# Kernel optimization log

Hardware: AMD Instinct MI355X
Metric: run time of the kernel (lower is better)

Reference implementation:

```python
import jax, jax.numpy as jnp
import numpy as np

T, N, E = 64, 50000, 1600000
DYN, STAT, GH, RH = 1, 6, 32, 64


def setup_inputs() -> dict:
    key = jax.random.key(0)
    ks = jax.random.split(key, 12)
    s = 0.05
    return {
        "dyn_seq": jax.random.normal(ks[0], (T, N, DYN), jnp.float32),
        "static": jax.random.normal(ks[1], (N, STAT), jnp.float32),
        "edge_index": jax.random.randint(ks[2], (2, E), 0, N, jnp.int32),
        "gcn_w0": s * jax.random.normal(ks[3], (DYN + STAT, GH), jnp.float32),
        "gcn_b0": jnp.zeros((GH,), jnp.float32),
        "gcn_w1": s * jax.random.normal(ks[4], (GH, GH), jnp.float32),
        "gcn_b1": jnp.zeros((GH,), jnp.float32),
        "w_ih": s * jax.random.normal(ks[5], (3 * RH, GH), jnp.float32),
        "w_hh": s * jax.random.normal(ks[6], (3 * RH, RH), jnp.float32),
        "b_ih": jnp.zeros((3 * RH,), jnp.float32),
        "b_hh": jnp.zeros((3 * RH,), jnp.float32),
        "mlp_w1": s * jax.random.normal(ks[7], (RH, RH), jnp.float32),
        "mlp_b1": jnp.zeros((RH,), jnp.float32),
        "mlp_w2": s * jax.random.normal(ks[8], (1, RH), jnp.float32),
        "mlp_b2": jnp.zeros((1,), jnp.float32),
    }


def reference(dyn_seq, static, edge_index, gcn_w0, gcn_b0, gcn_w1, gcn_b1,
              w_ih, w_hh, b_ih, b_hh, mlp_w1, mlp_b1, mlp_w2, mlp_b2):
    n = static.shape[0]
    # GCNConv normalization (PyG default): add self-loops, sym norm D^-1/2 (A+I) D^-1/2
    loops = jnp.arange(n, dtype=edge_index.dtype)
    src = jnp.concatenate([edge_index[0], loops])
    dst = jnp.concatenate([edge_index[1], loops])
    deg = jax.ops.segment_sum(jnp.ones_like(dst, jnp.float32), dst, num_segments=n)
    dinv = jnp.where(deg > 0, jax.lax.rsqrt(deg), 0.0)
    norm = (dinv[src] * dinv[dst])[:, None]  # [E+N, 1]

    def gcn(h, w, b):
        h = h @ w  # transform first (small feature dim), then aggregate
        agg = jax.ops.segment_sum(h[src] * norm, dst, num_segments=n)
        return jax.nn.relu(agg + b)

    def step(x_t):  # x_t: [N, DYN]
        x = jnp.concatenate([x_t, static], axis=1)
        return gcn(gcn(x, gcn_w0, gcn_b0), gcn_w1, gcn_b1)

    H = jax.lax.map(step, dyn_seq)  # [T, N, GH] (sequential over T to bound memory)

    rh = w_hh.shape[1]

    def gru_step(h, x_t):  # torch nn.GRU cell math
        gx = x_t @ w_ih.T + b_ih
        gh = h @ w_hh.T + b_hh
        xr, xz, xn = jnp.split(gx, 3, axis=-1)
        hr, hz, hn = jnp.split(gh, 3, axis=-1)
        r = jax.nn.sigmoid(xr + hr)
        z = jax.nn.sigmoid(xz + hz)
        cand = jnp.tanh(xn + r * hn)
        h_new = (1.0 - z) * cand + z * h
        return h_new, None

    h0 = jnp.zeros((n, rh), H.dtype)
    h_last, _ = jax.lax.scan(gru_step, h0, H)  # last GRU output == out[:, -1, :]
    hid = jax.nn.relu(h_last @ mlp_w1.T + mlp_b1)
    return (hid @ mlp_w2.T + mlp_b2).squeeze(-1)  # [N]
```

## Files before the change

### kernel.cpp

```cpp
#include <hip/hip_runtime.h>
#include <hip/hip_bf16.h>

#define T_   64
#define N_   50000
#define E_   1600000
#define GH_  32
#define RH_  64
#define TB32_ 32
#define G32B_ 12500
#define GB_  782
#define NB_  196
#define AB_  12500

typedef _Float16 half_t;
typedef __attribute__((ext_vector_type(8))) _Float16 half8;
typedef __attribute__((ext_vector_type(4))) _Float16 half4;
typedef __attribute__((ext_vector_type(4))) float f32x4;
typedef __attribute__((ext_vector_type(4))) int i32x4;

static __device__ __forceinline__ float fast_sigmoid(float v) {
    float e = __expf(-v);
    return __builtin_amdgcn_rcpf(1.0f + e);
}
static __device__ __forceinline__ float fast_tanh(float v) {
    return 2.0f * fast_sigmoid(2.0f * v) - 1.0f;
}


__global__ __launch_bounds__(256)
void k_transpose(const float* __restrict__ dyn, half_t* __restrict__ dynT) {
    __shared__ float tile[64][65];
    int n0 = blockIdx.x * 64;
    int tx = threadIdx.x, ty = threadIdx.y;
#pragma unroll
    for (int r = 0; r < 16; ++r) {
        int t = r * 4 + ty;
        int n = n0 + tx;
        tile[t][tx] = (n < N_) ? dyn[(size_t)t * N_ + n] : 0.0f;
    }
    __syncthreads();
#pragma unroll
    for (int r = 0; r < 16; ++r) {
        int nl = r * 4 + ty;
        int n = n0 + nl;
        if (n < N_) dynT[(size_t)n * 64 + tx] = (half_t)tile[tx][nl];
    }
}

__global__ void k_hist(const int* __restrict__ src, const int* __restrict__ dst,
                       int* __restrict__ cnt) {
    int e = blockIdx.x * blockDim.x + threadIdx.x;
    if (e >= E_) return;
    atomicAdd(&cnt[dst[e] * 16 + (src[e] >> 12)], 1);
}

__global__ __launch_bounds__(256)
void k_scanA(const int* __restrict__ cnt, int* __restrict__ deg,
             int* __restrict__ row_ptr, int* __restrict__ bsum) {
    __shared__ int buf[256];
    int tid = threadIdx.x;
    int i = blockIdx.x * 256 + tid;
    int v = 0;
    if (i < N_) {
        const int4* c4 = (const int4*)(cnt + i * 16);
#pragma unroll
        for (int c = 0; c < 4; ++c) {
            int4 w = c4[c];
            v += w.x + w.y + w.z + w.w;
        }
        deg[i] = v;
    }
    buf[tid] = v;
    __syncthreads();
#pragma unroll
    for (int off = 1; off < 256; off <<= 1) {
        int t = (tid >= off) ? buf[tid - off] : 0;
        __syncthreads();
        buf[tid] += t;
        __syncthreads();
    }
    if (i < N_) row_ptr[i + 1] = buf[tid];
    if (tid == 255) bsum[blockIdx.x] = buf[255];
}
__global__ __launch_bounds__(256)
void k_scanB(int* __restrict__ bsum, int nb) {
    __shared__ int buf[256];
    int tid = threadIdx.x;
    buf[tid] = (tid < nb) ? bsum[tid] : 0;
    __syncthreads();
#pragma unroll
    for (int off = 1; off < 256; off <<= 1) {
        int t = (tid >= off) ? buf[tid - off] : 0;
        __syncthreads();
        buf[tid] += t;
        __syncthreads();
    }
    if (tid < nb) bsum[tid] = (tid > 0) ? buf[tid - 1] : 0;
}
__global__ __launch_bounds__(256)
void k_scanC(int* __restrict__ row_ptr, const int* __restrict__ bsum) {
    int i = blockIdx.x * 256 + threadIdx.x;
    if (i == 0) row_ptr[0] = 0;
    if (i < N_) row_ptr[i + 1] += bsum[blockIdx.x];
}

__global__ __launch_bounds__(256)
void k_rowscan(const int* __restrict__ row_ptr, int* __restrict__ cnt,
               int* __restrict__ rp2) {
    int n = blockIdx.x * 256 + threadIdx.x;
    if (n >= N_) return;
    int run = row_ptr[n];
#pragma unroll
    for (int t = 0; t < 16; ++t) {
        int c = cnt[n * 16 + t];
        rp2[n * 16 + t] = run;
        run += c;
        cnt[n * 16 + t] = 0;
    }
}

__global__ __launch_bounds__(256)
void k_node_init(const int* __restrict__ deg,
                 const float* __restrict__ statics,
                 const float* __restrict__ w0,
                 float* __restrict__ dinv,
                 float* __restrict__ selfn,
                 half_t* __restrict__ h0s) {
    int n = blockIdx.x * blockDim.x + threadIdx.x;
    if (n >= N_) return;
    float d  = (float)deg[n] + 1.0f;
    float di = rsqrtf(d);
    dinv[n] = di;
    selfn[n] = di * di;
    float s[6];
#pragma unroll
    for (int j = 0; j < 6; ++j) s[j] = statics[n * 6 + j];
    half8 o[4];
#pragma unroll
    for (int k = 0; k < GH_; ++k) {
        float v = 0.0f;
#pragma unroll
        for (int j = 0; j < 6; ++j) v += s[j] * w0[(1 + j) * GH_ + k];
        o[k >> 3][k & 7] = (half_t)v;
    }
    half8* dst8 = (half8*)(h0s + (size_t)n * GH_);
#pragma unroll
    for (int c = 0; c < 4; ++c) dst8[c] = o[c];
}

__global__ void k_scatter2(const int* __restrict__ src, const int* __restrict__ dst,
                           const float* __restrict__ dinv,
                           const int* __restrict__ rp2, int* __restrict__ cnt,
                           int2* __restrict__ erec) {
    int e = blockIdx.x * blockDim.x + threadIdx.x;
    if (e >= E_) return;
    int s = src[e], d = dst[e];
    int slot = d * 16 + (s >> 12);
    int pos = rp2[slot] + atomicAdd(&cnt[slot], 1);
    erec[pos] = make_int2(s, __float_as_int(dinv[s] * dinv[d]));
}

__global__ void k_wB(const float* __restrict__ wih, const float* __restrict__ whh,
                     half_t* __restrict__ wB) {
    int idx = blockIdx.x * 256 + threadIdx.x;
    if (idx >= 96 * 192) return;
    int j = idx & 7;
    int r = idx >> 3;
    int m = r & 15; r >>= 4;
    int q = r & 3;  r >>= 2;
    int nt = r % 12;
    int c = r / 12;
    int k = c * 32 + q * 8 + j;
    int col = nt * 16 + m;
    float v = (k < 32) ? wih[col * 32 + k] : whh[col * 64 + (k - 32)];
    wB[idx] = (half_t)v;
}

__global__ void k_w1B(const float* __restrict__ w1, half_t* __restrict__ w1B) {
    int idx = blockIdx.x * 256 + threadIdx.x;
    if (idx >= 1024) return;
    int j = idx & 7;
    int m = (idx >> 3) & 15;
    int q = (idx >> 7) & 3;
    int nt = idx >> 9;
    w1B[idx] = (half_t)w1[(q * 8 + j) * GH_ + nt * 16 + m];
}


static __device__ __forceinline__
void aall_body(int bid, const int* __restrict__ row_ptr, const int2* __restrict__ erec,
               const float* __restrict__ selfn, const half_t* __restrict__ dynT,
               half_t* __restrict__ aTh) {
    int wv = __builtin_amdgcn_readfirstlane(threadIdx.x >> 6);
    int n = bid * 4 + wv;
    int lane = threadIdx.x & 63;
    float acc = selfn[n] * (float)dynT[(size_t)n * 64 + lane];
    int e0 = row_ptr[n], e1 = row_ptr[n + 1];
    int e = e0;
    for (; e < e1 && (e & 3); ++e) {
        int2 r = erec[e];
        acc += __int_as_float(r.y) * (float)dynT[(size_t)r.x * 64 + lane];
    }
    for (; e + 4 <= e1; e += 4) {
        int4 p0 = *(const int4*)(erec + e);
        int4 p1 = *(const int4*)(erec + e + 2);
        float v0 = (float)dynT[(size_t)p0.x * 64 + lane];
        float v1 = (float)dynT[(size_t)p0.z * 64 + lane];
        float v2 = (float)dynT[(size_t)p1.x * 64 + lane];
        float v3 = (float)dynT[(size_t)p1.z * 64 + lane];
        acc += __int_as_float(p0.y) * v0 + __int_as_float(p0.w) * v1
             + __int_as_float(p1.y) * v2 + __int_as_float(p1.w) * v3;
    }
    for (; e < e1; ++e) {
        int2 r = erec[e];
        acc += __int_as_float(r.y) * (float)dynT[(size_t)r.x * 64 + lane];
    }
    aTh[(size_t)n * 64 + lane] = (half_t)acc;
}

static __device__ __forceinline__
void g16s_body(int bid, const int* __restrict__ row_ptr, const int2* __restrict__ erec,
               const float* __restrict__ selfn, const half_t* __restrict__ h0s,
               const float* __restrict__ b0, half_t* __restrict__ ch) {
    int gid = bid * 256 + threadIdx.x;
    int n = gid >> 2, q = gid & 3;
    if (n >= N_) return;
    const half8* f8 = (const half8*)h0s;
    float acc[8];
    {
        half8 sv = f8[(size_t)n * 4 + q];
        float sn = selfn[n];
#pragma unroll
        for (int i = 0; i < 8; ++i) acc[i] = sn * (float)sv[i];
    }
    int e0 = row_ptr[n], e1 = row_ptr[n + 1];
    int e = e0;
    for (; e < e1 && (e & 3); ++e) {
        int2 r = erec[e];
        float nm = __int_as_float(r.y);
        half8 v = f8[(size_t)r.x * 4 + q];
#pragma unroll
        for (int i = 0; i < 8; ++i) acc[i] += nm * (float)v[i];
    }
    for (; e + 4 <= e1; e += 4) {
        int4 p0 = *(const int4*)(erec + e);
        int4 p1 = *(const int4*)(erec + e + 2);
        half8 v0 = f8[(size_t)p0.x * 4 + q];
        half8 v1 = f8[(size_t)p0.z * 4 + q];
        half8 v2 = f8[(size_t)p1.x * 4 + q];
        half8 v3 = f8[(size_t)p1.z * 4 + q];
        float n0 = __int_as_float(p0.y), n1 = __int_as_float(p0.w);
        float n2 = __int_as_float(p1.y), n3 = __int_as_float(p1.w);
#pragma unroll
        for (int i = 0; i < 8; ++i)
            acc[i] += n0 * (float)v0[i] + n1 * (float)v1[i]
                    + n2 * (float)v2[i] + n3 * (float)v3[i];
    }
    for (; e < e1; ++e) {
        int2 r = erec[e];
        float nm = __int_as_float(r.y);
        half8 v = f8[(size_t)r.x * 4 + q];
#pragma unroll
        for (int i = 0; i < 8; ++i) acc[i] += nm * (float)v[i];
    }
    half8 o;
#pragma unroll
    for (int i = 0; i < 8; ++i) o[i] = (half_t)(acc[i] + b0[q * 8 + i]);
    *(half8*)(ch + (size_t)n * GH_ + q * 8) = o;
}

__global__ __launch_bounds__(256)
void k_aux(const int* __restrict__ row_ptr, const int2* __restrict__ erec,
           const float* __restrict__ selfn, const half_t* __restrict__ dynT,
           half_t* __restrict__ aTh, const half_t* __restrict__ h0s,
           const float* __restrict__ b0, half_t* __restrict__ ch) {
    if ((int)blockIdx.x < AB_)
        aall_body(blockIdx.x, row_ptr, erec, selfn, dynT, aTh);
    else
        g16s_body((int)blockIdx.x - AB_, row_ptr, erec, selfn, h0s, b0, ch);
}

__global__ __launch_bounds__(256)
void k_gather32(const int* __restrict__ row_ptr, const int2* __restrict__ erec,
                const float* __restrict__ selfn,
                const half_t* __restrict__ aTh,
                const half_t* __restrict__ ch,
                const float* __restrict__ w0,
                const half_t* __restrict__ w1B,
                const float* __restrict__ b1,
                half_t* __restrict__ xblk,
                int h) {
    __shared__ half_t sh[4 * 32 * 40];
    int tid = threadIdx.x;
    int wv = __builtin_amdgcn_readfirstlane(tid >> 6);
    int n = blockIdx.x * 4 + wv;
    int l = tid & 63;
    int tg = l >> 3;
    int tg4 = tg * 4;
    int kc = (l & 7) * 4;
    float w0r[4];
#pragma unroll
    for (int i = 0; i < 4; ++i) w0r[i] = w0[kc + i];

    const half_t* aBase = aTh + h * 32 + tg4;
    float acc[4][4];

    auto edge_acc = [&](half4 aa, half4 cc, float nmv) {
#pragma unroll
        for (int tt = 0; tt < 4; ++tt) {
#pragma unroll
            for (int i = 0; i < 4; ++i) {
                float hv = fmaxf(fmaf((float)aa[tt], w0r[i], (float)cc[i]), 0.0f);
                acc[tt][i] = fmaf(nmv, hv, acc[tt][i]);
            }
        }
    };

    {
        float sn = selfn[n];
        half4 a4 = *(const half4*)(aBase + (size_t)n * 64);
        half4 c4 = *(const half4*)(ch + (size_t)n * GH_ + kc);
#pragma unroll
        for (int tt = 0; tt < 4; ++tt) {
#pragma unroll
            for (int i = 0; i < 4; ++i) {
                float hv = fmaxf(fmaf((float)a4[tt], w0r[i], (float)c4[i]), 0.0f);
                acc[tt][i] = sn * hv;
            }
        }
    }

    int e0 = row_ptr[n], e1 = row_ptr[n + 1];
    int e = e0;
    if (e < e1 && (e & 1)) {
        int2 r = erec[e];
        half4 a4 = *(const half4*)(aBase + (size_t)r.x * 64);
        half4 c4 = *(const half4*)(ch + (size_t)r.x * GH_ + kc);
        edge_acc(a4, c4, __int_as_float(r.y));
        ++e;
    }
    for (; e + 4 <= e1; e += 4) {
        i32x4 p0 = *(const i32x4*)(erec + e);
        i32x4 p1 = *(const i32x4*)(erec + e + 2);
        size_t s0 = (size_t)p0[0], s1 = (size_t)p0[2];
        size_t s2 = (size_t)p1[0], s3 = (size_t)p1[2];
        half4 a40 = *(const half4*)(aBase + s0 * 64);
        half4 a41 = *(const half4*)(aBase + s1 * 64);
        half4 a42 = *(const half4*)(aBase + s2 * 64);
        half4 a43 = *(const half4*)(aBase + s3 * 64);
        half4 c40 = *(const half4*)(ch + s0 * GH_ + kc);
        half4 c41 = *(const half4*)(ch + s1 * GH_ + kc);
        half4 c42 = *(const half4*)(ch + s2 * GH_ + kc);
        half4 c43 = *(const half4*)(ch + s3 * GH_ + kc);
        edge_acc(a40, c40, __int_as_float(p0[1]));
        edge_acc(a41, c41, __int_as_float(p0[3]));
        edge_acc(a42, c42, __int_as_float(p1[1]));
        edge_acc(a43, c43, __int_as_float(p1[3]));
    }
    for (; e < e1; ++e) {
        int2 r = erec[e];
        half4 a4 = *(const half4*)(aBase + (size_t)r.x * 64);
        half4 c4 = *(const half4*)(ch + (size_t)r.x * GH_ + kc);
        edge_acc(a4, c4, __int_as_float(r.y));
    }

    half_t* shw = sh + wv * 32 * 40;
#pragma unroll
    for (int tt = 0; tt < 4; ++tt) {
        half4 o;
#pragma unroll
        for (int i = 0; i < 4; ++i) o[i] = (half_t)acc[tt][i];
        *(half4*)(shw + (tg4 + tt) * 40 + kc) = o;
    }

    int c16 = l & 15, q = l >> 4;
    const half8* wB8 = (const half8*)w1B;
    half8 bf0 = wB8[(0 * 4 + q) * 16 + c16];
    half8 bf1 = wB8[(1 * 4 + q) * 16 + c16];
    float b1v0 = b1[c16], b1v1 = b1[16 + c16];

    const f32x4 zero = {0.0f, 0.0f, 0.0f, 0.0f};
    half8 A0 = *(const half8*)(shw + (0 * 16 + c16) * 40 + q * 8);
    half8 A1 = *(const half8*)(shw + (1 * 16 + c16) * 40 + q * 8);
    f32x4 C00 = __builtin_amdgcn_mfma_f32_16x16x32_f16(A0, bf0, zero, 0, 0, 0);
    f32x4 C01 = __builtin_amdgcn_mfma_f32_16x16x32_f16(A0, bf1, zero, 0, 0, 0);
    f32x4 C10 = __builtin_amdgcn_mfma_f32_16x16x32_f16(A1, bf0, zero, 0, 0, 0);
    f32x4 C11 = __builtin_amdgcn_mfma_f32_16x16x32_f16(A1, bf1, zero, 0, 0, 0);

#pragma unroll
    for (int reg = 0; reg < 4; ++reg) {
        shw[(q * 4 + reg) * 40 + c16]           = (half_t)fmaxf(C00[reg] + b1v0, 0.0f);
        shw[(q * 4 + reg) * 40 + 16 + c16]      = (half_t)fmaxf(C01[reg] + b1v1, 0.0f);
        shw[(16 + q * 4 + reg) * 40 + c16]      = (half_t)fmaxf(C10[reg] + b1v0, 0.0f);
        shw[(16 + q * 4 + reg) * 40 + 16 + c16] = (half_t)fmaxf(C11[reg] + b1v1, 0.0f);
    }

#pragma unroll
    for (int i = 0; i < 2; ++i) {
        int idx = i * 64 + l;
        int tl = idx >> 2;
        int kcol = (idx & 3) * 8;
        half8 v = *(const half8*)(shw + tl * 40 + kcol);
        *(half8*)(xblk + ((size_t)tl * N_ + n) * GH_ + kcol) = v;
    }
}

#define HSTR_ 72
__global__ __launch_bounds__(256, 2)
void k_gru32(const half_t* __restrict__ xblk,
             const half_t* __restrict__ wB,
             const float* __restrict__ bih, const float* __restrict__ bhh,
             half_t* __restrict__ hA) {
    __shared__ half_t hL[64 * HSTR_];
    int tid = threadIdx.x;
    int nb0 = blockIdx.x * 64;
    for (int i = tid; i < 64 * 8; i += 256) {
        int node = i >> 3, ch = i & 7;
        half8 v = *(const half8*)(hA + (size_t)(nb0 + node) * RH_ + ch * 8);
        *(half8*)(hL + node * HSTR_ + ch * 8) = v;
    }
    __syncthreads();
    int lane = tid & 63;
    int wv = tid >> 6;
    int c16 = lane & 15, q = lane >> 4;
    const half8* wB8 = (const half8*)wB;
    half8 bfr[3][12];
#pragma unroll
    for (int c = 0; c < 3; ++c)
#pragma unroll
        for (int nt = 0; nt < 12; ++nt)
            bfr[c][nt] = wB8[((c * 12 + nt) * 4 + q) * 16 + c16];
    float br[4], bz[4], bnx[4], bnh[4];
#pragma unroll
    for (int jt = 0; jt < 4; ++jt) {
        int j = jt * 16 + c16;
        br[jt]  = bih[j] + bhh[j];
        bz[jt]  = bih[64 + j] + bhh[64 + j];
        bnx[jt] = bih[128 + j];
        bnh[jt] = bhh[128 + j];
    }
    int mrow = wv * 16 + c16;
    const half_t* hrow = hL + mrow * HSTR_;
    half_t hreg[4][4];
#pragma unroll
    for (int jt = 0; jt < 4; ++jt)
#pragma unroll
        for (int reg = 0; reg < 4; ++reg)
            hreg[jt][reg] = hL[(wv * 16 + q * 4 + reg) * HSTR_ + jt * 16 + c16];
    const f32x4 zero = {0.0f, 0.0f, 0.0f, 0.0f};
#pragma unroll 1
    for (int u = 0; u < TB32_; ++u) {
        half8 ax = __builtin_nontemporal_load(
            (const half8*)(xblk + ((size_t)u * N_ + nb0 + mrow) * GH_ + q * 8));
        half8 ah0 = *(const half8*)(hrow + q * 8);
        half8 ah1 = *(const half8*)(hrow + 32 + q * 8);
        f32x4 Crz[8], Cnx[4], Cnh[4];
#pragma unroll
        for (int nt = 0; nt < 8; ++nt) {
            Crz[nt] = __builtin_amdgcn_mfma_f32_16x16x32_f16(ax,  bfr[0][nt], zero,     0, 0, 0);
            Crz[nt] = __builtin_amdgcn_mfma_f32_16x16x32_f16(ah0, bfr[1][nt], Crz[nt], 0, 0, 0);
            Crz[nt] = __builtin_amdgcn_mfma_f32_16x16x32_f16(ah1, bfr[2][nt], Crz[nt], 0, 0, 0);
        }
#pragma unroll
        for (int nt = 0; nt < 4; ++nt) {
            Cnx[nt] = __builtin_amdgcn_mfma_f32_16x16x32_f16(ax,  bfr[0][8 + nt], zero,     0, 0, 0);
            Cnh[nt] = __builtin_amdgcn_mfma_f32_16x16x32_f16(ah0, bfr[1][8 + nt], zero,     0, 0, 0);
            Cnh[nt] = __builtin_amdgcn_mfma_f32_16x16x32_f16(ah1, bfr[2][8 + nt], Cnh[nt], 0, 0, 0);
        }
#pragma unroll
        for (int jt = 0; jt < 4; ++jt) {
#pragma unroll
            for (int reg = 0; reg < 4; ++reg) {
                int nl = wv * 16 + q * 4 + reg;
                int jj = jt * 16 + c16;
                float hold = (float)hreg[jt][reg];
                float r  = fast_sigmoid(Crz[jt][reg] + br[jt]);
                float z  = fast_sigmoid(Crz[4 + jt][reg] + bz[jt]);
                float cd = fast_tanh(Cnx[jt][reg] + bnx[jt] + r * (Cnh[jt][reg] + bnh[jt]));
                half_t hnew = (half_t)((1.0f - z) * cd + z * hold);
                hreg[jt][reg] = hnew;
                hL[nl * HSTR_ + jj] = hnew;
            }
        }
    }
    __syncthreads();
    for (int i = tid; i < 64 * 8; i += 256) {
        int node = i >> 3, ch = i & 7;
        half8 v = *(const half8*)(hL + node * HSTR_ + ch * 8);
        *(half8*)(hA + (size_t)(nb0 + node) * RH_ + ch * 8) = v;
    }
}

__global__ __launch_bounds__(256)
void k_mlp(const half_t* __restrict__ hA, const float* __restrict__ w1,
           const float* __restrict__ b1, const float* __restrict__ w2,
           const float* __restrict__ b2, float* __restrict__ out) {
    int n = blockIdx.x * blockDim.x + threadIdx.x;
    if (n >= N_) return;
    float h[RH_];
    const half8* h8 = (const half8*)(hA + (size_t)n * RH_);
#pragma unroll
    for (int c = 0; c < 8; ++c) {
        half8 v = h8[c];
#pragma unroll
        for (int i = 0; i < 8; ++i) h[c * 8 + i] = (float)v[i];
    }
    float acc = b2[0];
#pragma unroll 1
    for (int j = 0; j < RH_; ++j) {
        float v = b1[j];
#pragma unroll
        for (int k = 0; k < RH_; ++k) v += w1[j * RH_ + k] * h[k];
        v = v > 0.0f ? v : 0.0f;
        acc += w2[j] * v;
    }
    out[n] = acc;
}

extern "C" void kernel_launch(void* const* d_in, const int* in_sizes, int n_in,
                              void* d_out, int out_size, void* d_ws, size_t ws_size,
                              hipStream_t stream) {
    const float* dyn     = (const float*)d_in[0];
    const float* statics = (const float*)d_in[1];
    const int*   ei      = (const int*)d_in[2];
    const float* w0      = (const float*)d_in[3];
    const float* b0      = (const float*)d_in[4];
    const float* w1      = (const float*)d_in[5];
    const float* b1      = (const float*)d_in[6];
    const float* wih     = (const float*)d_in[7];
    const float* whh     = (const float*)d_in[8];
    const float* bih     = (const float*)d_in[9];
    const float* bhh     = (const float*)d_in[10];
    const float* mw1     = (const float*)d_in[11];
    const float* mb1     = (const float*)d_in[12];
    const float* mw2     = (const float*)d_in[13];
    const float* mb2     = (const float*)d_in[14];
    const int* src = ei;
    const int* dst = ei + E_;

    char* ws = (char*)d_ws;
    auto alloc = [&](size_t elems) {
        elems = (elems + 63) & ~(size_t)63;
        void* p = ws; ws += elems * 4; return p;
    };
    const int NPAD = N_ + 64;
    int*    deg     = (int*)alloc(N_);
    int*    row_ptr = (int*)alloc(N_ + 4);
    int*    bsum    = (int*)alloc(256);
    int*    cnt     = (int*)alloc((size_t)N_ * 16);
    int*    rp2     = (int*)alloc((size_t)N_ * 16);
    int2*   erec    = (int2*)alloc((size_t)E_ * 2);
    float*  dinv    = (float*)alloc(N_);
    float*  selfn   = (float*)alloc(N_);
    half_t* h0s     = (half_t*)alloc((size_t)N_ * GH_ / 2);
    half_t* ch      = (half_t*)alloc((size_t)N_ * GH_ / 2);
    half_t* aTh     = (half_t*)alloc((size_t)N_ * 64 / 2);
    half_t* xblk    = (half_t*)alloc(((size_t)32 * N_ + 64) * GH_ / 2);
    half_t* hA      = (half_t*)alloc((size_t)NPAD * RH_ / 2);
    half_t* dynT    = (half_t*)alloc((size_t)N_ * 64 / 2);
    half_t* wB      = (half_t*)alloc(96 * 192 / 2);
    half_t* w1B     = (half_t*)alloc(1024 / 2);

    auto cdiv = [](long long x, int b) { return (unsigned)((x + b - 1) / b); };
    const int B = 256;

    hipMemsetAsync(cnt, 0, (size_t)N_ * 16 * sizeof(int), stream);
    hipMemsetAsync(hA, 0, (size_t)NPAD * RH_ * sizeof(half_t), stream);

    k_transpose<<<cdiv(N_, 64), dim3(64, 4), 0, stream>>>(dyn, dynT);
    k_hist<<<cdiv(E_, B), B, 0, stream>>>(src, dst, cnt);
    k_scanA<<<NB_, B, 0, stream>>>(cnt, deg, row_ptr, bsum);
    k_scanB<<<1, B, 0, stream>>>(bsum, NB_);
    k_scanC<<<NB_, B, 0, stream>>>(row_ptr, bsum);
    k_rowscan<<<NB_, B, 0, stream>>>(row_ptr, cnt, rp2);
    k_node_init<<<NB_, B, 0, stream>>>(deg, statics, w0, dinv, selfn, h0s);
    k_scatter2<<<cdiv(E_, B), B, 0, stream>>>(src, dst, dinv, rp2, cnt, erec);
    k_wB<<<cdiv(96 * 192, B), B, 0, stream>>>(wih, whh, wB);
    k_w1B<<<4, B, 0, stream>>>(w1, w1B);
    k_aux<<<AB_ + GB_, B, 0, stream>>>(row_ptr, erec, selfn, dynT, aTh, h0s, b0, ch);

    for (int h = 0; h < 2; ++h) {
        k_gather32<<<G32B_, B, 0, stream>>>(row_ptr, erec, selfn, aTh, ch, w0,
                                            w1B, b1, xblk, h);
        k_gru32<<<GB_, B, 0, stream>>>(xblk, wB, bih, bhh, hA);
    }
    k_mlp<<<NB_, B, 0, stream>>>(hA, mw1, mb1, mw2, mb2, (float*)d_out);
}
```

Before: 938.4 us.

## Gather all 64 timesteps in one pass when workspace permits

Adds a k_gather64 kernel that processes all 64 timesteps per node in a single edge traversal. The edge records, the ch row and the neighbor indices are now loaded once rather than once per half, and the xblk buffer is sized for all 64 timesteps. The GRU kernel then runs twice over the two halves of this buffer. The cost is double the register accumulators (acc[8][4]), which may lower occupancy, and a larger workspace. If the workspace is too small, the code falls back to the old two-pass path.

After: 939.2 us. About the same (+0.1%).

```diff
diff --git a/kernel.cpp b/kernel.cpp
--- a/kernel.cpp
+++ b/kernel.cpp
@@ -281,6 +281,125 @@
 }
 
 __global__ __launch_bounds__(256)
+void k_gather64(const int* __restrict__ row_ptr, const int2* __restrict__ erec,
+                const float* __restrict__ selfn,
+                const half_t* __restrict__ aTh,
+                const half_t* __restrict__ ch,
+                const float* __restrict__ w0,
+                const half_t* __restrict__ w1B,
+                const float* __restrict__ b1,
+                half_t* __restrict__ xblk) {
+    __shared__ half_t sh[4 * 64 * 40];
+    int tid = threadIdx.x;
+    int wv = __builtin_amdgcn_readfirstlane(tid >> 6);
+    int n = blockIdx.x * 4 + wv;
+    int l = tid & 63;
+    int tg8 = (l >> 3) * 8;
+    int kc = (l & 7) * 4;
+    float w0r[4];
+#pragma unroll
+    for (int i = 0; i < 4; ++i) w0r[i] = w0[kc + i];
+
+    const half_t* aBase = aTh + tg8;
+    float acc[8][4];
+
+    auto edge_acc = [&](half8 aa, half4 cc, float nmv) {
+#pragma unroll
+        for (int tt = 0; tt < 8; ++tt) {
+#pragma unroll
+            for (int i = 0; i < 4; ++i) {
+                float hv = fmaxf(fmaf((float)aa[tt], w0r[i], (float)cc[i]), 0.0f);
+                acc[tt][i] = fmaf(nmv, hv, acc[tt][i]);
+            }
+        }
+    };
+
+    {
+        float sn = selfn[n];
+        half8 a8 = *(const half8*)(aBase + (size_t)n * 64);
+        half4 c4 = *(const half4*)(ch + (size_t)n * GH_ + kc);
+#pragma unroll
+        for (int tt = 0; tt < 8; ++tt) {
+#pragma unroll
+            for (int i = 0; i < 4; ++i) {
+                float hv = fmaxf(fmaf((float)a8[tt], w0r[i], (float)c4[i]), 0.0f);
+                acc[tt][i] = sn * hv;
+            }
+        }
+    }
+
+    int e0 = row_ptr[n], e1 = row_ptr[n + 1];
+    int e = e0;
+    if (e < e1 && (e & 1)) {
+        int2 r = erec[e];
+        half8 a8 = *(const half8*)(aBase + (size_t)r.x * 64);
+        half4 c4 = *(const half4*)(ch + (size_t)r.x * GH_ + kc);
+        edge_acc(a8, c4, __int_as_float(r.y));
+        ++e;
+    }
+    for (; e + 2 <= e1; e += 2) {
+        i32x4 p0 = *(const i32x4*)(erec + e);
+        size_t s0 = (size_t)p0[0], s1 = (size_t)p0[2];
+        half8 a80 = *(const half8*)(aBase + s0 * 64);
+        half8 a81 = *(const half8*)(aBase + s1 * 64);
+        half4 c40 = *(const half4*)(ch + s0 * GH_ + kc);
+        half4 c41 = *(const half4*)(ch + s1 * GH_ + kc);
+        edge_acc(a80, c40, __int_as_float(p0[1]));
+        edge_acc(a81, c41, __int_as_float(p0[3]));
+    }
+    for (; e < e1; ++e) {
+        int2 r = erec[e];
+        half8 a8 = *(const half8*)(aBase + (size_t)r.x * 64);
+        half4 c4 = *(const half4*)(ch + (size_t)r.x * GH_ + kc);
+        edge_acc(a8, c4, __int_as_float(r.y));
+    }
+
+    half_t* shw = sh + wv * 64 * 40;
+#pragma unroll
+    for (int tt = 0; tt < 8; ++tt) {
+        half4 o;
+#pragma unroll
+        for (int i = 0; i < 4; ++i) o[i] = (half_t)acc[tt][i];
+        *(half4*)(shw + (tg8 + tt) * 40 + kc) = o;
+    }
+
+    int c16 = l & 15, q = l >> 4;
+    const half8* wB8 = (const half8*)w1B;
+    half8 bf0 = wB8[(0 * 4 + q) * 16 + c16];
+    half8 bf1 = wB8[(1 * 4 + q) * 16 + c16];
+    float b1v0 = b1[c16], b1v1 = b1[16 + c16];
+
+    const f32x4 zero = {0.0f, 0.0f, 0.0f, 0.0f};
+    half8 A[4];
+#pragma unroll
+    for (int b = 0; b < 4; ++b)
+        A[b] = *(const half8*)(shw + (b * 16 + c16) * 40 + q * 8);
+    f32x4 C0[4], C1[4];
+#pragma unroll
+    for (int b = 0; b < 4; ++b) {
+        C0[b] = __builtin_amdgcn_mfma_f32_16x16x32_f16(A[b], bf0, zero, 0, 0, 0);
+        C1[b] = __builtin_amdgcn_mfma_f32_16x16x32_f16(A[b], bf1, zero, 0, 0, 0);
+    }
+#pragma unroll
+    for (int b = 0; b < 4; ++b)
+#pragma unroll
+        for (int reg = 0; reg < 4; ++reg) {
+            int row = b * 16 + q * 4 + reg;
+            shw[row * 40 + c16]      = (half_t)fmaxf(C0[b][reg] + b1v0, 0.0f);
+            shw[row * 40 + 16 + c16] = (half_t)fmaxf(C1[b][reg] + b1v1, 0.0f);
+        }
+
+#pragma unroll
+    for (int i = 0; i < 4; ++i) {
+        int idx = i * 64 + l;
+        int tl = idx >> 2;
+        int kcol = (idx & 3) * 8;
+        half8 v = *(const half8*)(shw + tl * 40 + kcol);
+        *(half8*)(xblk + ((size_t)tl * N_ + n) * GH_ + kcol) = v;
+    }
+}
+
+__global__ __launch_bounds__(256)
 void k_gather32(const int* __restrict__ row_ptr, const int2* __restrict__ erec,
                 const float* __restrict__ selfn,
                 const half_t* __restrict__ aTh,
@@ -295,25 +414,22 @@
     int wv = __builtin_amdgcn_readfirstlane(tid >> 6);
     int n = blockIdx.x * 4 + wv;
     int l = tid & 63;
-    int tg = l >> 3;
-    int tg4 = tg * 4;
+    int tg4 = (l >> 3) * 4;
     int kc = (l & 7) * 4;
     float w0r[4];
 #pragma unroll
     for (int i = 0; i < 4; ++i) w0r[i] = w0[kc + i];
-
     const half_t* aBase = aTh + h * 32 + tg4;
     float acc[4][4];
 
     auto edge_acc = [&](half4 aa, half4 cc, float nmv) {
 #pragma unroll
-        for (int tt = 0; tt < 4; ++tt) {
+        for (int tt = 0; tt < 4; ++tt)
 #pragma unroll
             for (int i = 0; i < 4; ++i) {
                 float hv = fmaxf(fmaf((float)aa[tt], w0r[i], (float)cc[i]), 0.0f);
                 acc[tt][i] = fmaf(nmv, hv, acc[tt][i]);
             }
-        }
     };
 
     {
@@ -321,13 +437,12 @@
         half4 a4 = *(const half4*)(aBase + (size_t)n * 64);
         half4 c4 = *(const half4*)(ch + (size_t)n * GH_ + kc);
 #pragma unroll
-        for (int tt = 0; tt < 4; ++tt) {
+        for (int tt = 0; tt < 4; ++tt)
 #pragma unroll
             for (int i = 0; i < 4; ++i) {
                 float hv = fmaxf(fmaf((float)a4[tt], w0r[i], (float)c4[i]), 0.0f);
                 acc[tt][i] = sn * hv;
             }
-        }
     }
 
     int e0 = row_ptr[n], e1 = row_ptr[n + 1];
@@ -386,7 +501,6 @@
     f32x4 C01 = __builtin_amdgcn_mfma_f32_16x16x32_f16(A0, bf1, zero, 0, 0, 0);
     f32x4 C10 = __builtin_amdgcn_mfma_f32_16x16x32_f16(A1, bf0, zero, 0, 0, 0);
     f32x4 C11 = __builtin_amdgcn_mfma_f32_16x16x32_f16(A1, bf1, zero, 0, 0, 0);
-
 #pragma unroll
     for (int reg = 0; reg < 4; ++reg) {
         shw[(q * 4 + reg) * 40 + c16]           = (half_t)fmaxf(C00[reg] + b1v0, 0.0f);
@@ -394,7 +508,6 @@
         shw[(16 + q * 4 + reg) * 40 + c16]      = (half_t)fmaxf(C10[reg] + b1v0, 0.0f);
         shw[(16 + q * 4 + reg) * 40 + 16 + c16] = (half_t)fmaxf(C11[reg] + b1v1, 0.0f);
     }
-
 #pragma unroll
     for (int i = 0; i < 2; ++i) {
         int idx = i * 64 + l;
@@ -555,11 +668,14 @@
     half_t* h0s     = (half_t*)alloc((size_t)N_ * GH_ / 2);
     half_t* ch      = (half_t*)alloc((size_t)N_ * GH_ / 2);
     half_t* aTh     = (half_t*)alloc((size_t)N_ * 64 / 2);
-    half_t* xblk    = (half_t*)alloc(((size_t)32 * N_ + 64) * GH_ / 2);
     half_t* hA      = (half_t*)alloc((size_t)NPAD * RH_ / 2);
     half_t* dynT    = (half_t*)alloc((size_t)N_ * 64 / 2);
     half_t* wB      = (half_t*)alloc(96 * 192 / 2);
     half_t* w1B     = (half_t*)alloc(1024 / 2);
+    size_t used = (size_t)(ws - (char*)d_ws);
+    size_t xblk64_bytes = ((size_t)64 * N_ + 64) * GH_ * sizeof(half_t);
+    bool use64 = (ws_size >= used + xblk64_bytes + 4096);
+    half_t* xblk = (half_t*)ws;
 
     auto cdiv = [](long long x, int b) { return (unsigned)((x + b - 1) / b); };
     const int B = 256;
@@ -579,10 +695,17 @@
     k_w1B<<<4, B, 0, stream>>>(w1, w1B);
     k_aux<<<AB_ + GB_, B, 0, stream>>>(row_ptr, erec, selfn, dynT, aTh, h0s, b0, ch);
 
-    for (int h = 0; h < 2; ++h) {
-        k_gather32<<<G32B_, B, 0, stream>>>(row_ptr, erec, selfn, aTh, ch, w0,
-                                            w1B, b1, xblk, h);
+    if (use64) {
+        k_gather64<<<G32B_, B, 0, stream>>>(row_ptr, erec, selfn, aTh, ch, w0,
+                                            w1B, b1, xblk);
         k_gru32<<<GB_, B, 0, stream>>>(xblk, wB, bih, bhh, hA);
+        k_gru32<<<GB_, B, 0, stream>>>(xblk + (size_t)32 * N_ * GH_, wB, bih, bhh, hA);
+    } else {
+        for (int h = 0; h < 2; ++h) {
+            k_gather32<<<G32B_, B, 0, stream>>>(row_ptr, erec, selfn, aTh, ch, w0,
+                                                w1B, b1, xblk, h);
+            k_gru32<<<GB_, B, 0, stream>>>(xblk, wB, bih, bhh, hA);
+        }
     }
     k_mlp<<<NB_, B, 0, stream>>>(hA, mw1, mb1, mw2, mb2, (float*)d_out);
 }
```
